# Optimization experiments

Measured on AMD Instinct MI355X. Metric: run time of the kernel, lower is better.

Reference implementation:

```python
import jax, jax.numpy as jnp
import numpy as np
import math

D_MODEL = 512
NUM_HEADS = 8
B, S = 2, 4096


def setup_inputs() -> dict:
    key = jax.random.key(0)
    ks = jax.random.split(key, 11)
    d = D_MODEL
    sc = 1.0 / math.sqrt(d)
    return {
        "query": jax.random.normal(ks[0], (B, S, d), jnp.float32),
        "key": jax.random.normal(ks[1], (B, S, d), jnp.float32),
        "value": jax.random.normal(ks[2], (B, S, d), jnp.float32),
        "Wq": jax.random.normal(ks[3], (d, d), jnp.float32) * sc,
        "bq": jnp.zeros((d,), jnp.float32),
        "Wk": jax.random.normal(ks[4], (d, d), jnp.float32) * sc,
        "bk": jnp.zeros((d,), jnp.float32),
        "Wv": jax.random.normal(ks[5], (d, d), jnp.float32) * sc,
        "bv": jnp.zeros((d,), jnp.float32),
        "Wo": jax.random.normal(ks[6], (d, d), jnp.float32) * sc,
        "bo": jnp.zeros((d,), jnp.float32),
    }


def reference(query, key, value, Wq, bq, Wk, bk, Wv, bv, Wo, bo):
    b, q_len, d_model = query.shape
    k_len = key.shape[1]
    h = NUM_HEADS
    d_k = d_model // h
    q = (query @ Wq.T + bq).reshape(b, q_len, h, d_k)
    k = (key @ Wk.T + bk).reshape(b, k_len, h, d_k)
    v = (value @ Wv.T + bv).reshape(b, k_len, h, d_k)
    # NOTE: faithful to source — softmax WITHOUT pre-scaling, then divide by sqrt(d_k)
    comp = jnp.einsum('bqhd,bkhd->bhqk', q, k)
    attn = jax.nn.softmax(comp, axis=-1) / jnp.sqrt(jnp.asarray(d_k, comp.dtype))
    x = jnp.einsum('bhqk,bkhd->bqhd', attn, v)
    return x.reshape(b, q_len, d_model) @ Wo.T + bo
```

## Files before the change

kernel.cpp:

```cpp
#include <hip/hip_runtime.h>

typedef _Float16 f16;
typedef __fp16 fp16x2 __attribute__((ext_vector_type(2)));
typedef _Float16 half4 __attribute__((ext_vector_type(4)));
typedef _Float16 half8 __attribute__((ext_vector_type(8)));
typedef float f32x4 __attribute__((ext_vector_type(4)));
typedef float float4v __attribute__((ext_vector_type(4)));

#define LOG2E 1.44269504088896340736f

__device__ __forceinline__ half8 cat8(half4 a, half4 b) {
    half8 r;
    r[0] = a[0]; r[1] = a[1]; r[2] = a[2]; r[3] = a[3];
    r[4] = b[0]; r[5] = b[1]; r[6] = b[2]; r[7] = b[3];
    return r;
}

union H8 { fp16x2 h2[4]; half8 h8; };

#define TR8(baddr, d0,d1,d2,d3,d4,d5,d6,d7)                                   \
  asm volatile("ds_read_b64_tr_b16 %0, %8 offset:0\n\t"                       \
               "ds_read_b64_tr_b16 %1, %8 offset:512\n\t"                     \
               "ds_read_b64_tr_b16 %2, %8 offset:128\n\t"                     \
               "ds_read_b64_tr_b16 %3, %8 offset:640\n\t"                     \
               "ds_read_b64_tr_b16 %4, %8 offset:256\n\t"                     \
               "ds_read_b64_tr_b16 %5, %8 offset:768\n\t"                     \
               "ds_read_b64_tr_b16 %6, %8 offset:384\n\t"                     \
               "ds_read_b64_tr_b16 %7, %8 offset:896"                         \
               : "=&v"(d0),"=&v"(d1),"=&v"(d2),"=&v"(d3),                     \
                 "=&v"(d4),"=&v"(d5),"=&v"(d6),"=&v"(d7)                      \
               : "v"(baddr) : "memory")

#define LGKM0_FENCE()                                                          \
  do { asm volatile("s_waitcnt lgkmcnt(0)" ::: "memory");                      \
       __builtin_amdgcn_sched_barrier(0); } while (0)

__device__ __forceinline__ float rowmax16(const f32x4 sf[4]) {
    float a = fmaxf(fmaxf(sf[0][0], sf[0][1]), fmaxf(sf[0][2], sf[0][3]));
    float b = fmaxf(fmaxf(sf[1][0], sf[1][1]), fmaxf(sf[1][2], sf[1][3]));
    float c = fmaxf(fmaxf(sf[2][0], sf[2][1]), fmaxf(sf[2][2], sf[2][3]));
    float d = fmaxf(fmaxf(sf[3][0], sf[3][1]), fmaxf(sf[3][2], sf[3][3]));
    return fmaxf(fmaxf(a, b), fmaxf(c, d));
}

__device__ __forceinline__ void max_defer(
    const f32x4 sf[4], float& mL, f32x4 o[4], f32x4& la)
{
    float vm = rowmax16(sf);
    vm = fmaxf(vm, __shfl_xor(vm, 16, 64));
    vm = fmaxf(vm, __shfl_xor(vm, 32, 64));
    float vmL = vm * LOG2E;
    if (__any(vmL > mL + 8.0f)) {
        float mn = fmaxf(mL, vmL);
        float al = __builtin_amdgcn_exp2f(mL - mn);
        la *= al;
        #pragma unroll
        for (int db = 0; db < 4; ++db) o[db] *= al;
        mL = mn;
    }
}

__device__ __forceinline__ void exp_pack(
    const f32x4 sf[4], float mL, H8& pb0, H8& pb1)
{
    float pe[16];
    #pragma unroll
    for (int kb = 0; kb < 4; ++kb)
        #pragma unroll
        for (int ro = 0; ro < 4; ++ro)
            pe[kb * 4 + ro] = __builtin_amdgcn_exp2f(fmaf(sf[kb][ro], LOG2E, -mL));
    pb0.h2[0] = __builtin_amdgcn_cvt_pkrtz(pe[0],  pe[1]);
    pb0.h2[1] = __builtin_amdgcn_cvt_pkrtz(pe[2],  pe[3]);
    pb0.h2[2] = __builtin_amdgcn_cvt_pkrtz(pe[4],  pe[5]);
    pb0.h2[3] = __builtin_amdgcn_cvt_pkrtz(pe[6],  pe[7]);
    pb1.h2[0] = __builtin_amdgcn_cvt_pkrtz(pe[8],  pe[9]);
    pb1.h2[1] = __builtin_amdgcn_cvt_pkrtz(pe[10], pe[11]);
    pb1.h2[2] = __builtin_amdgcn_cvt_pkrtz(pe[12], pe[13]);
    pb1.h2[3] = __builtin_amdgcn_cvt_pkrtz(pe[14], pe[15]);
}

__global__ __launch_bounds__(256) void qkv_proj(
    const float* __restrict__ Aq, const float* __restrict__ Ak, const float* __restrict__ Av,
    const float* __restrict__ Wq, const float* __restrict__ Wk, const float* __restrict__ Wv,
    const float* __restrict__ bq, const float* __restrict__ bk, const float* __restrict__ bv,
    f16* __restrict__ Qh, f16* __restrict__ Kh, f16* __restrict__ Vh)
{
    const int z = blockIdx.z;
    const float* __restrict__ A    = (z == 0) ? Aq : (z == 1) ? Ak : Av;
    const float* __restrict__ W    = (z == 0) ? Wq : (z == 1) ? Wk : Wv;
    const float* __restrict__ bias = (z == 0) ? bq : (z == 1) ? bk : bv;
    f16* __restrict__ dst          = (z == 0) ? Qh : (z == 1) ? Kh : Vh;

    __shared__ __align__(16) f16 As[128 * 40];
    __shared__ __align__(16) f16 Ws[128 * 40];

    const int t  = threadIdx.x;
    const int m0 = blockIdx.y * 128;
    const int n0 = blockIdx.x * 128;
    const int w = t >> 6, lane = t & 63, lr = lane & 15, lg = lane >> 4;
    const int wr = w >> 1, wc = w & 1;

    f32x4 acc[4][4] = {};

    for (int k0 = 0; k0 < 512; k0 += 32) {
        #pragma unroll
        for (int it = 0; it < 2; ++it) {
            int c = t + it * 256;
            int row  = c >> 2;
            int col8 = (c & 3) * 8;

            const float* ga = A + (size_t)(m0 + row) * 512 + k0 + col8;
            float4v a0 = *(const float4v*)ga;
            float4v a1 = *(const float4v*)(ga + 4);
            half8 ha;
            ha[0] = (f16)a0[0]; ha[1] = (f16)a0[1]; ha[2] = (f16)a0[2]; ha[3] = (f16)a0[3];
            ha[4] = (f16)a1[0]; ha[5] = (f16)a1[1]; ha[6] = (f16)a1[2]; ha[7] = (f16)a1[3];
            *(half8*)&As[row * 40 + col8] = ha;

            const float* gw = W + (size_t)(n0 + row) * 512 + k0 + col8;
            float4v w0 = *(const float4v*)gw;
            float4v w1 = *(const float4v*)(gw + 4);
            half8 hw;
            hw[0] = (f16)w0[0]; hw[1] = (f16)w0[1]; hw[2] = (f16)w0[2]; hw[3] = (f16)w0[3];
            hw[4] = (f16)w1[0]; hw[5] = (f16)w1[1]; hw[6] = (f16)w1[2]; hw[7] = (f16)w1[3];
            *(half8*)&Ws[row * 40 + col8] = hw;
        }
        __syncthreads();

        half8 af[4], bf[4];
        #pragma unroll
        for (int i = 0; i < 4; ++i) {
            af[i] = *(const half8*)&As[(wr * 64 + i * 16 + lr) * 40 + lg * 8];
            bf[i] = *(const half8*)&Ws[(wc * 64 + i * 16 + lr) * 40 + lg * 8];
        }
        #pragma unroll
        for (int mi = 0; mi < 4; ++mi)
            #pragma unroll
            for (int ni = 0; ni < 4; ++ni)
                acc[mi][ni] = __builtin_amdgcn_mfma_f32_16x16x32_f16(af[mi], bf[ni], acc[mi][ni], 0, 0, 0);
        __syncthreads();
    }

    #pragma unroll
    for (int mi = 0; mi < 4; ++mi) {
        #pragma unroll
        for (int ni = 0; ni < 4; ++ni) {
            int col = n0 + wc * 64 + ni * 16 + lr;
            float bv_ = bias[col];
            int h  = col >> 6;
            int dd = col & 63;
            #pragma unroll
            for (int r = 0; r < 4; ++r) {
                int row = m0 + wr * 64 + mi * 16 + lg * 4 + r;
                int b = row >> 12;
                int s = row & 4095;
                dst[(((size_t)(b * 8 + h)) * 4096 + s) * 64 + dd] = (f16)(acc[mi][ni][r] + bv_);
            }
        }
    }
}

__global__ __launch_bounds__(256, 2) void flash_attn(
    const f16* __restrict__ Qh, const f16* __restrict__ Kh, const f16* __restrict__ Vh,
    f16* __restrict__ Xh)
{
    const int bh  = blockIdx.y;
    const int t = threadIdx.x, w = t >> 6, lane = t & 63, lr = lane & 15, lg = lane >> 4;
    const int q0 = blockIdx.x * 128 + w * 32;

    __shared__ __align__(16) f16 Ks[2][64 * 72];
    __shared__ __align__(16) f16 Vs[2][64 * 64];

    const size_t hb = (size_t)bh * (4096 * 64);

    half8 aq00 = *(const half8*)&Qh[hb + (size_t)(q0 + lr) * 64 + lg * 8];
    half8 aq01 = *(const half8*)&Qh[hb + (size_t)(q0 + lr) * 64 + 32 + lg * 8];
    half8 aq10 = *(const half8*)&Qh[hb + (size_t)(q0 + 16 + lr) * 64 + lg * 8];
    half8 aq11 = *(const half8*)&Qh[hb + (size_t)(q0 + 16 + lr) * 64 + 32 + lg * 8];

    half8 ones;
    #pragma unroll
    for (int j = 0; j < 8; ++j) ones[j] = (f16)1.0f;
    const f32x4 zf = {0.0f, 0.0f, 0.0f, 0.0f};

    const int srow = t >> 3;
    const int scol = (t & 7) * 8;
    const int kdstA = srow * 72 + scol;
    const int kdstB = kdstA + 32 * 72;
    const int vdstA = ((((srow >> 2) & 3) * 16) + (srow >> 4) * 4 + (scol >> 4)) * 64
                    + (srow & 3) * 16 + (scol & 15);
    const int vdstB = vdstA + 512;

    f32x4 o0[4] = {}, o1[4] = {};
    f32x4 la0 = {}, la1 = {};
    float mL0 = -INFINITY, mL1 = -INFINITY;

    const f16* kbase = Kh + hb + (size_t)srow * 64 + scol;
    const f16* vbase = Vh + hb + (size_t)srow * 64 + scol;

    half8 kregA = *(const half8*)kbase;
    half8 kregB = *(const half8*)(kbase + 2048);
    half8 vregA = *(const half8*)vbase;
    half8 vregB = *(const half8*)(vbase + 2048);

    for (int kt = 0; kt < 4096; kt += 64) {
        const int bi = (kt >> 6) & 1;
        f16* ks = &Ks[bi][0];
        f16* vs = &Vs[bi][0];

        *(half8*)&ks[kdstA] = kregA;
        *(half8*)&ks[kdstB] = kregB;
        *(half8*)&vs[vdstA] = vregA;
        *(half8*)&vs[vdstB] = vregB;
        __syncthreads();

        int koff = ((kt + 64) & 4095) << 6;
        kregA = *(const half8*)(kbase + koff);
        kregB = *(const half8*)(kbase + 2048 + koff);
        vregA = *(const half8*)(vbase + koff);
        vregB = *(const half8*)(vbase + 2048 + koff);

        f32x4 sf0[4], sf1[4];
        {
            half8 kf[4];
            #pragma unroll
            for (int kb = 0; kb < 4; ++kb)
                kf[kb] = *(const half8*)&ks[(kb * 16 + lr) * 72 + lg * 8];
            __builtin_amdgcn_s_setprio(1);
            #pragma unroll
            for (int kb = 0; kb < 4; ++kb)
                sf0[kb] = __builtin_amdgcn_mfma_f32_16x16x32_f16(kf[kb], aq00, zf, 0, 0, 0);
            #pragma unroll
            for (int kb = 0; kb < 4; ++kb)
                sf1[kb] = __builtin_amdgcn_mfma_f32_16x16x32_f16(kf[kb], aq10, zf, 0, 0, 0);
            __builtin_amdgcn_s_setprio(0);
            #pragma unroll
            for (int kb = 0; kb < 4; ++kb)
                kf[kb] = *(const half8*)&ks[(kb * 16 + lr) * 72 + 32 + lg * 8];
            __builtin_amdgcn_s_setprio(1);
            #pragma unroll
            for (int kb = 0; kb < 4; ++kb)
                sf0[kb] = __builtin_amdgcn_mfma_f32_16x16x32_f16(kf[kb], aq01, sf0[kb], 0, 0, 0);
            #pragma unroll
            for (int kb = 0; kb < 4; ++kb)
                sf1[kb] = __builtin_amdgcn_mfma_f32_16x16x32_f16(kf[kb], aq11, sf1[kb], 0, 0, 0);
            __builtin_amdgcn_s_setprio(0);
        }

        max_defer(sf0, mL0, o0, la0);
        max_defer(sf1, mL1, o1, la1);

        const unsigned vb = (unsigned)(size_t)vs + (unsigned)(lg * 2048 + lr * 8);
        half4 ua0,ua1,ua2,ua3,ua4,ua5,ua6,ua7;
        half4 ub0,ub1,ub2,ub3,ub4,ub5,ub6,ub7;
        TR8(vb,         ua0,ua1,ua2,ua3,ua4,ua5,ua6,ua7);
        TR8(vb + 1024u, ub0,ub1,ub2,ub3,ub4,ub5,ub6,ub7);

        H8 p00, p01, p10, p11;
        exp_pack(sf0, mL0, p00, p01);
        exp_pack(sf1, mL1, p10, p11);

        LGKM0_FENCE();

        __builtin_amdgcn_s_setprio(1);
        o0[0] = __builtin_amdgcn_mfma_f32_16x16x32_f16(cat8(ua0,ua1), p00.h8, o0[0], 0, 0, 0);
        o0[1] = __builtin_amdgcn_mfma_f32_16x16x32_f16(cat8(ua2,ua3), p00.h8, o0[1], 0, 0, 0);
        o0[2] = __builtin_amdgcn_mfma_f32_16x16x32_f16(cat8(ua4,ua5), p00.h8, o0[2], 0, 0, 0);
        o0[3] = __builtin_amdgcn_mfma_f32_16x16x32_f16(cat8(ua6,ua7), p00.h8, o0[3], 0, 0, 0);
        o1[0] = __builtin_amdgcn_mfma_f32_16x16x32_f16(cat8(ua0,ua1), p10.h8, o1[0], 0, 0, 0);
        o1[1] = __builtin_amdgcn_mfma_f32_16x16x32_f16(cat8(ua2,ua3), p10.h8, o1[1], 0, 0, 0);
        o1[2] = __builtin_amdgcn_mfma_f32_16x16x32_f16(cat8(ua4,ua5), p10.h8, o1[2], 0, 0, 0);
        o1[3] = __builtin_amdgcn_mfma_f32_16x16x32_f16(cat8(ua6,ua7), p10.h8, o1[3], 0, 0, 0);
        la0 = __builtin_amdgcn_mfma_f32_16x16x32_f16(ones, p00.h8, la0, 0, 0, 0);
        la1 = __builtin_amdgcn_mfma_f32_16x16x32_f16(ones, p10.h8, la1, 0, 0, 0);
        o0[0] = __builtin_amdgcn_mfma_f32_16x16x32_f16(cat8(ub0,ub1), p01.h8, o0[0], 0, 0, 0);
        o0[1] = __builtin_amdgcn_mfma_f32_16x16x32_f16(cat8(ub2,ub3), p01.h8, o0[1], 0, 0, 0);
        o0[2] = __builtin_amdgcn_mfma_f32_16x16x32_f16(cat8(ub4,ub5), p01.h8, o0[2], 0, 0, 0);
        o0[3] = __builtin_amdgcn_mfma_f32_16x16x32_f16(cat8(ub6,ub7), p01.h8, o0[3], 0, 0, 0);
        o1[0] = __builtin_amdgcn_mfma_f32_16x16x32_f16(cat8(ub0,ub1), p11.h8, o1[0], 0, 0, 0);
        o1[1] = __builtin_amdgcn_mfma_f32_16x16x32_f16(cat8(ub2,ub3), p11.h8, o1[1], 0, 0, 0);
        o1[2] = __builtin_amdgcn_mfma_f32_16x16x32_f16(cat8(ub4,ub5), p11.h8, o1[2], 0, 0, 0);
        o1[3] = __builtin_amdgcn_mfma_f32_16x16x32_f16(cat8(ub6,ub7), p11.h8, o1[3], 0, 0, 0);
        la0 = __builtin_amdgcn_mfma_f32_16x16x32_f16(ones, p01.h8, la0, 0, 0, 0);
        la1 = __builtin_amdgcn_mfma_f32_16x16x32_f16(ones, p11.h8, la1, 0, 0, 0);
        __builtin_amdgcn_s_setprio(0);
    }

    const int b = bh >> 3, h = bh & 7;
    const float inv0 = 1.0f / (la0[0] * 8.0f);
    const float inv1 = 1.0f / (la1[0] * 8.0f);
    const int q0_ = q0 + lr, q1_ = q0 + 16 + lr;
    #pragma unroll
    for (int db = 0; db < 4; ++db) {
        half4 hv0, hv1;
        hv0[0] = (f16)(o0[db][0] * inv0);
        hv0[1] = (f16)(o0[db][1] * inv0);
        hv0[2] = (f16)(o0[db][2] * inv0);
        hv0[3] = (f16)(o0[db][3] * inv0);
        *(half4*)&Xh[((size_t)(b * 4096 + q0_)) * 512 + h * 64 + db * 16 + lg * 4] = hv0;
        hv1[0] = (f16)(o1[db][0] * inv1);
        hv1[1] = (f16)(o1[db][1] * inv1);
        hv1[2] = (f16)(o1[db][2] * inv1);
        hv1[3] = (f16)(o1[db][3] * inv1);
        *(half4*)&Xh[((size_t)(b * 4096 + q1_)) * 512 + h * 64 + db * 16 + lg * 4] = hv1;
    }
}

__global__ __launch_bounds__(256) void out_proj(
    const f16* __restrict__ Xh, const float* __restrict__ Wo, const float* __restrict__ bo,
    float* __restrict__ out)
{
    __shared__ __align__(16) f16 As[128 * 40];
    __shared__ __align__(16) f16 Ws[128 * 40];

    const int t  = threadIdx.x;
    const int m0 = blockIdx.y * 128;
    const int n0 = blockIdx.x * 128;
    const int w = t >> 6, lane = t & 63, lr = lane & 15, lg = lane >> 4;
    const int wr = w >> 1, wc = w & 1;

    f32x4 acc[4][4] = {};

    for (int k0 = 0; k0 < 512; k0 += 32) {
        #pragma unroll
        for (int it = 0; it < 2; ++it) {
            int c = t + it * 256;
            int row  = c >> 2;
            int col8 = (c & 3) * 8;

            *(half8*)&As[row * 40 + col8] =
                *(const half8*)&Xh[(size_t)(m0 + row) * 512 + k0 + col8];

            const float* gw = Wo + (size_t)(n0 + row) * 512 + k0 + col8;
            float4v w0 = *(const float4v*)gw;
            float4v w1 = *(const float4v*)(gw + 4);
            half8 hw;
            hw[0] = (f16)w0[0]; hw[1] = (f16)w0[1]; hw[2] = (f16)w0[2]; hw[3] = (f16)w0[3];
            hw[4] = (f16)w1[0]; hw[5] = (f16)w1[1]; hw[6] = (f16)w1[2]; hw[7] = (f16)w1[3];
            *(half8*)&Ws[row * 40 + col8] = hw;
        }
        __syncthreads();

        half8 af[4], bf[4];
        #pragma unroll
        for (int i = 0; i < 4; ++i) {
            af[i] = *(const half8*)&As[(wr * 64 + i * 16 + lr) * 40 + lg * 8];
            bf[i] = *(const half8*)&Ws[(wc * 64 + i * 16 + lr) * 40 + lg * 8];
        }
        #pragma unroll
        for (int mi = 0; mi < 4; ++mi)
            #pragma unroll
            for (int ni = 0; ni < 4; ++ni)
                acc[mi][ni] = __builtin_amdgcn_mfma_f32_16x16x32_f16(af[mi], bf[ni], acc[mi][ni], 0, 0, 0);
        __syncthreads();
    }

    #pragma unroll
    for (int mi = 0; mi < 4; ++mi) {
        #pragma unroll
        for (int ni = 0; ni < 4; ++ni) {
            int col = n0 + wc * 64 + ni * 16 + lr;
            float bb = bo[col];
            #pragma unroll
            for (int r = 0; r < 4; ++r) {
                int row = m0 + wr * 64 + mi * 16 + lg * 4 + r;
                out[(size_t)row * 512 + col] = acc[mi][ni][r] + bb;
            }
        }
    }
}

extern "C" void kernel_launch(void* const* d_in, const int* in_sizes, int n_in,
                              void* d_out, int out_size, void* d_ws, size_t ws_size,
                              hipStream_t stream) {
    const float* query = (const float*)d_in[0];
    const float* key   = (const float*)d_in[1];
    const float* value = (const float*)d_in[2];
    const float* Wq    = (const float*)d_in[3];
    const float* bq    = (const float*)d_in[4];
    const float* Wk    = (const float*)d_in[5];
    const float* bk    = (const float*)d_in[6];
    const float* Wv    = (const float*)d_in[7];
    const float* bv    = (const float*)d_in[8];
    const float* Wo    = (const float*)d_in[9];
    const float* bo    = (const float*)d_in[10];
    float* out = (float*)d_out;

    char* ws = (char*)d_ws;
    f16* Qh = (f16*)(ws);
    f16* Kh = (f16*)(ws + 8388608);
    f16* Vh = (f16*)(ws + 16777216);
    f16* Xh = (f16*)(ws + 25165824);

    qkv_proj<<<dim3(4, 64, 3), 256, 0, stream>>>(query, key, value,
                                                 Wq, Wk, Wv, bq, bk, bv,
                                                 Qh, Kh, Vh);
    flash_attn<<<dim3(32, 16), 256, 0, stream>>>(Qh, Kh, Vh, Xh);
    out_proj<<<dim3(4, 64), 256, 0, stream>>>(Xh, Wo, bo, out);
}
```

Before: 164.6 us.

## Split attention along key dimension into two halves and merge with combine kernel

Launches flash attention with a z dimension of 2, so each block processes half of the key/value sequence and writes unnormalized-by-8 partial outputs plus per-row max and sum. A new combine kernel merges the two halves with log-sum-exp weights and applies the 1/sqrt(d_k) scaling. This doubles the grid from 512 to 1024 blocks to fill more CUs, and raises the occupancy hint in launch bounds. The cost is an extra kernel launch, extra global traffic for the partial outputs and statistics, and fp16 rounding of the partial results.

```diff
diff --git a/kernel.cpp b/kernel.cpp
--- a/kernel.cpp
+++ b/kernel.cpp
@@ -6,6 +6,7 @@
 typedef _Float16 half8 __attribute__((ext_vector_type(8)));
 typedef float f32x4 __attribute__((ext_vector_type(4)));
 typedef float float4v __attribute__((ext_vector_type(4)));
+typedef float float2v __attribute__((ext_vector_type(2)));
 
 #define LOG2E 1.44269504088896340736f
 
@@ -160,11 +161,12 @@
     }
 }
 
-__global__ __launch_bounds__(256, 2) void flash_attn(
+__global__ __launch_bounds__(256, 4) void flash_attn(
     const f16* __restrict__ Qh, const f16* __restrict__ Kh, const f16* __restrict__ Vh,
-    f16* __restrict__ Xh)
+    f16* __restrict__ Xp, float2v* __restrict__ mlp)
 {
     const int bh  = blockIdx.y;
+    const int z   = blockIdx.z;
     const int t = threadIdx.x, w = t >> 6, lane = t & 63, lr = lane & 15, lg = lane >> 4;
     const int q0 = blockIdx.x * 128 + w * 32;
 
@@ -195,15 +197,15 @@
     f32x4 la0 = {}, la1 = {};
     float mL0 = -INFINITY, mL1 = -INFINITY;
 
-    const f16* kbase = Kh + hb + (size_t)srow * 64 + scol;
-    const f16* vbase = Vh + hb + (size_t)srow * 64 + scol;
+    const f16* kbase = Kh + hb + (size_t)(z * 2048 + srow) * 64 + scol;
+    const f16* vbase = Vh + hb + (size_t)(z * 2048 + srow) * 64 + scol;
 
     half8 kregA = *(const half8*)kbase;
     half8 kregB = *(const half8*)(kbase + 2048);
     half8 vregA = *(const half8*)vbase;
     half8 vregB = *(const half8*)(vbase + 2048);
 
-    for (int kt = 0; kt < 4096; kt += 64) {
+    for (int kt = 0; kt < 2048; kt += 64) {
         const int bi = (kt >> 6) & 1;
         f16* ks = &Ks[bi][0];
         f16* vs = &Vs[bi][0];
@@ -214,7 +216,7 @@
         *(half8*)&vs[vdstB] = vregB;
         __syncthreads();
 
-        int koff = ((kt + 64) & 4095) << 6;
+        int koff = ((kt + 64) & 2047) << 6;
         kregA = *(const half8*)(kbase + koff);
         kregB = *(const half8*)(kbase + 2048 + koff);
         vregA = *(const half8*)(vbase + koff);
@@ -287,8 +289,9 @@
     }
 
     const int b = bh >> 3, h = bh & 7;
-    const float inv0 = 1.0f / (la0[0] * 8.0f);
-    const float inv1 = 1.0f / (la1[0] * 8.0f);
+    f16* X = Xp + (size_t)z * (8192 * 512);
+    const float inv0 = 1.0f / la0[0];
+    const float inv1 = 1.0f / la1[0];
     const int q0_ = q0 + lr, q1_ = q0 + 16 + lr;
     #pragma unroll
     for (int db = 0; db < 4; ++db) {
@@ -297,13 +300,48 @@
         hv0[1] = (f16)(o0[db][1] * inv0);
         hv0[2] = (f16)(o0[db][2] * inv0);
         hv0[3] = (f16)(o0[db][3] * inv0);
-        *(half4*)&Xh[((size_t)(b * 4096 + q0_)) * 512 + h * 64 + db * 16 + lg * 4] = hv0;
+        *(half4*)&X[((size_t)(b * 4096 + q0_)) * 512 + h * 64 + db * 16 + lg * 4] = hv0;
         hv1[0] = (f16)(o1[db][0] * inv1);
         hv1[1] = (f16)(o1[db][1] * inv1);
         hv1[2] = (f16)(o1[db][2] * inv1);
         hv1[3] = (f16)(o1[db][3] * inv1);
-        *(half4*)&Xh[((size_t)(b * 4096 + q1_)) * 512 + h * 64 + db * 16 + lg * 4] = hv1;
-    }
+        *(half4*)&X[((size_t)(b * 4096 + q1_)) * 512 + h * 64 + db * 16 + lg * 4] = hv1;
+    }
+
+    if (lane < 16) {
+        float2v m0v; m0v[0] = mL0; m0v[1] = la0[0];
+        float2v m1v; m1v[0] = mL1; m1v[1] = la1[0];
+        mlp[(size_t)z * 65536 + bh * 4096 + q0_] = m0v;
+        mlp[(size_t)z * 65536 + bh * 4096 + q1_] = m1v;
+    }
+}
+
+__global__ __launch_bounds__(256) void combine_halves(
+    const f16* __restrict__ Xp, const float2v* __restrict__ mlp,
+    f16* __restrict__ Xh)
+{
+    const size_t idx  = (size_t)blockIdx.x * 256 + threadIdx.x;
+    const size_t flat = idx * 8;
+    const int h = (int)((flat >> 6) & 7);
+    const int s = (int)((flat >> 9) & 4095);
+    const int b = (int)(flat >> 21);
+    const int bhq = (b * 8 + h) * 4096 + s;
+
+    float2v ml1 = mlp[bhq];
+    float2v ml2 = mlp[65536 + bhq];
+    float mm = fmaxf(ml1[0], ml2[0]);
+    float a1 = __builtin_amdgcn_exp2f(ml1[0] - mm) * ml1[1];
+    float a2 = __builtin_amdgcn_exp2f(ml2[0] - mm) * ml2[1];
+    float inv = 1.0f / (8.0f * (a1 + a2));
+    float w1 = a1 * inv, w2 = a2 * inv;
+
+    half8 x1 = *(const half8*)&Xp[flat];
+    half8 x2 = *(const half8*)&Xp[(size_t)8192 * 512 + flat];
+    half8 r;
+    #pragma unroll
+    for (int j = 0; j < 8; ++j)
+        r[j] = (f16)(w1 * (float)x1[j] + w2 * (float)x2[j]);
+    *(half8*)&Xh[flat] = r;
 }
 
 __global__ __launch_bounds__(256) void out_proj(
@@ -387,14 +425,17 @@
     float* out = (float*)d_out;
 
     char* ws = (char*)d_ws;
-    f16* Qh = (f16*)(ws);
-    f16* Kh = (f16*)(ws + 8388608);
-    f16* Vh = (f16*)(ws + 16777216);
-    f16* Xh = (f16*)(ws + 25165824);
+    f16*     Qh  = (f16*)(ws);
+    f16*     Kh  = (f16*)(ws + 8388608);
+    f16*     Vh  = (f16*)(ws + 16777216);
+    f16*     Xp  = (f16*)(ws + 25165824);
+    float2v* mlp = (float2v*)(ws + 41943040);
+    f16*     Xh  = (f16*)(ws + 42991616);
 
     qkv_proj<<<dim3(4, 64, 3), 256, 0, stream>>>(query, key, value,
                                                  Wq, Wk, Wv, bq, bk, bv,
                                                  Qh, Kh, Vh);
-    flash_attn<<<dim3(32, 16), 256, 0, stream>>>(Qh, Kh, Vh, Xh);
+    flash_attn<<<dim3(32, 16, 2), 256, 0, stream>>>(Qh, Kh, Vh, Xp, mlp);
+    combine_halves<<<2048, 256, 0, stream>>>(Xp, mlp, Xh);
     out_proj<<<dim3(4, 64), 256, 0, stream>>>(Xh, Wo, bo, out);
 }
```

Result: slower. 307.6 us (+86.9%).
